# Kernel optimization log

Measured on AMD Instinct MI355X. Metric: run time of the kernel, lower is better.

## Reference

```python
import jax, jax.numpy as jnp
import numpy as np

TEMPERATURE = 0.0005

def conv1d(x, w, b):
    # x: [B,Cin,T], w: [Cout,Cin,K], 'same' padding as ConvNorm (pad=(K-1)//2)
    pad = (w.shape[-1] - 1) // 2
    y = jax.lax.conv_general_dilated(x, w, window_strides=(1,), padding=[(pad, pad)],
                                     dimension_numbers=('NCH', 'OIH', 'NCH'))
    return y + b[None, :, None]

def setup_inputs() -> dict:
    key = jax.random.key(0)
    ks = jax.random.split(key, 20)
    B, C_MEL, C_TXT, C_ATT, T1, T2 = 32, 80, 512, 80, 1600, 400
    s = 0.02
    return {
        'queries': jax.random.normal(ks[0], (B, C_MEL, T1), jnp.float32),
        'keys': jax.random.normal(ks[1], (B, C_TXT, T2), jnp.float32),
        'mask': jax.random.randint(ks[2], (B, T2, 1), 0, 2).astype(bool),
        'attn_prior': jax.random.uniform(ks[3], (B, T1, T2), jnp.float32),
        'speaker_embed': jax.random.normal(ks[4], (B, C_TXT), jnp.float32),
        # key_proj: Conv(512->1024,k3) -> ReLU -> Conv(1024->80,k1)
        'Wk1': jax.random.normal(ks[5], (C_TXT * 2, C_TXT, 3)) * s,
        'bk1': jax.random.normal(ks[6], (C_TXT * 2,)) * s,
        'Wk2': jax.random.normal(ks[7], (C_ATT, C_TXT * 2, 1)) * s,
        'bk2': jax.random.normal(ks[8], (C_ATT,)) * s,
        # query_proj: Conv(80->160,k3) -> ReLU -> Conv(160->80,k1) -> ReLU -> Conv(80->80,k1)
        'Wq1': jax.random.normal(ks[9], (C_MEL * 2, C_MEL, 3)) * s,
        'bq1': jax.random.normal(ks[10], (C_MEL * 2,)) * s,
        'Wq2': jax.random.normal(ks[11], (C_MEL, C_MEL * 2, 1)) * s,
        'bq2': jax.random.normal(ks[12], (C_MEL,)) * s,
        'Wq3': jax.random.normal(ks[13], (C_ATT, C_MEL, 1)) * s,
        'bq3': jax.random.normal(ks[14], (C_ATT,)) * s,
        # speaker projections (multi_speaker=True)
        'Wks': jax.random.normal(ks[15], (C_TXT, C_TXT)) * s,
        'bks': jax.random.normal(ks[16], (C_TXT,)) * s,
        'Wqs': jax.random.normal(ks[17], (C_MEL, C_TXT)) * s,
        'bqs': jax.random.normal(ks[18], (C_MEL,)) * s,
    }

def reference(queries, keys, mask, attn_prior, speaker_embed,
              Wk1, bk1, Wk2, bk2, Wq1, bq1, Wq2, bq2, Wq3, bq3,
              Wks, bks, Wqs, bqs):
    # speaker conditioning: Linear(spk) broadcast over time, added channelwise
    keys = keys + (speaker_embed @ Wks.T + bks)[:, :, None]
    queries = queries + (speaker_embed @ Wqs.T + bqs)[:, :, None]
    # projections
    k = jax.nn.relu(conv1d(keys, Wk1, bk1))
    k = conv1d(k, Wk2, bk2)                      # [B, C_att, T2]
    q = jax.nn.relu(conv1d(queries, Wq1, bq1))
    q = jax.nn.relu(conv1d(q, Wq2, bq2))
    q = conv1d(q, Wq3, bq3)                      # [B, C_att, T1]
    # -temp * sum_c (q-k)^2 == -temp * (||q||^2 + ||k||^2 - 2 q.k)
    q2 = jnp.sum(q * q, axis=1)                  # [B, T1]
    k2 = jnp.sum(k * k, axis=1)                  # [B, T2]
    qk = jnp.einsum('bct,bcs->bts', q, k)        # [B, T1, T2]
    attn = -TEMPERATURE * (q2[:, :, None] + k2[:, None, :] - 2.0 * qk)
    attn = attn[:, None]                         # [B, 1, T1, T2]
    attn = jax.nn.log_softmax(attn, axis=3) + jnp.log(attn_prior[:, None] + 1e-8)
    attn_logprob = attn
    m = jnp.transpose(mask, (0, 2, 1))[:, :, None, :]  # [B,1,1,T2]
    attn = jnp.where(m, -jnp.inf, attn)
    attn = jax.nn.softmax(attn, axis=3)
    return attn, attn_logprob
```

## Files before the change

kernel.cpp:

```cpp
#include <hip/hip_runtime.h>
#include <math.h>

#define TEMP 0.0005f
#define B_    32
#define CMEL  80
#define CTXT  512
#define T1_   1600
#define T2_   400

typedef short short8 __attribute__((ext_vector_type(8)));
typedef float f32x4 __attribute__((ext_vector_type(4)));

__device__ inline unsigned short f2bf(float f) {
    unsigned u = __float_as_uint(f);
    u += 0x7FFF + ((u >> 16) & 1);
    return (unsigned short)(u >> 16);
}
__device__ inline unsigned pack2(float a, float b) {
    return (unsigned)f2bf(a) | ((unsigned)f2bf(b) << 16);
}
__device__ inline float bf2f(unsigned short v) { return __uint_as_float(((unsigned)v) << 16); }

__global__ void bias_kernel(const float* __restrict__ se,
                            const float* __restrict__ Wks, const float* __restrict__ bks,
                            const float* __restrict__ Wqs, const float* __restrict__ bqs,
                            float* __restrict__ kb, float* __restrict__ qb) {
    int tid = blockIdx.x * blockDim.x + threadIdx.x;
    const int nk = B_ * CTXT;
    if (tid < nk) {
        int b = tid / CTXT, c = tid % CTXT;
        const float4* s4 = reinterpret_cast<const float4*>(se + b * CTXT);
        const float4* w4 = reinterpret_cast<const float4*>(Wks + (size_t)c * CTXT);
        float acc = bks[c];
        #pragma unroll 4
        for (int j = 0; j < CTXT / 4; ++j) {
            float4 a = s4[j], w = w4[j];
            acc += a.x * w.x + a.y * w.y + a.z * w.z + a.w * w.w;
        }
        kb[tid] = acc;
    } else if (tid < nk + B_ * CMEL) {
        int t = tid - nk;
        int b = t / CMEL, c = t % CMEL;
        const float4* s4 = reinterpret_cast<const float4*>(se + b * CTXT);
        const float4* w4 = reinterpret_cast<const float4*>(Wqs + (size_t)c * CTXT);
        float acc = bqs[c];
        #pragma unroll 4
        for (int j = 0; j < CTXT / 4; ++j) {
            float4 a = s4[j], w = w4[j];
            acc += a.x * w.x + a.y * w.y + a.z * w.z + a.w * w.w;
        }
        qb[t] = acc;
    }
}

__global__ void cast_weights_kernel(
        const float* __restrict__ Wk1, const float* __restrict__ Wk2,
        const float* __restrict__ Wq1, const float* __restrict__ Wq2,
        const float* __restrict__ Wq3,
        unsigned short* __restrict__ Ab1, unsigned short* __restrict__ A2,
        unsigned short* __restrict__ A3, unsigned short* __restrict__ A4,
        unsigned short* __restrict__ A5) {
    int e = blockIdx.x * 256 + threadIdx.x;
    const int n1 = 1572864, n2 = 81920, n3 = 46080, n4 = 12800, n5 = 7680;
    if (e < n1) {
        int co = e / 1536, rem = e - co * 1536;
        int dt = rem >> 9, ci = rem & 511;
        Ab1[e] = f2bf(Wk1[((size_t)co * 512 + ci) * 3 + dt]);
    } else if ((e -= n1) < n2) {
        A2[e] = f2bf(Wk2[e]);
    } else if ((e -= n2) < n3) {
        int co = e / 288, rem = e - co * 288;
        int dt = rem / 96, cc = rem - dt * 96;
        A3[e] = (cc < 80) ? f2bf(Wq1[((size_t)co * 80 + cc) * 3 + dt]) : 0;
    } else if ((e -= n3) < n4) {
        A4[e] = f2bf(Wq2[e]);
    } else if ((e -= n4) < n5) {
        int co = e / 96, cc = e - co * 96;
        A5[e] = (cc < 80) ? f2bf(Wq3[co * 80 + cc]) : 0;
    }
}

__global__ void castXk_kernel(const float* __restrict__ keys, const float* __restrict__ kb,
                              unsigned short* __restrict__ Xt) {
    __shared__ float tile[64][65];
    const int b = blockIdx.z;
    const int row0 = blockIdx.x * 64;
    const int ci0 = blockIdx.y * 64;
    const int tid = threadIdx.x;
    #pragma unroll
    for (int i = 0; i < 16; ++i) {
        int linear = i * 256 + tid;
        int ci_l = linear >> 6, t_l = linear & 63;
        int t = row0 + t_l - 1;
        float v = 0.f;
        if (t >= 0 && t < 400)
            v = keys[((size_t)b * 512 + ci0 + ci_l) * 400 + t] + kb[b * 512 + ci0 + ci_l];
        tile[t_l][ci_l] = v;
    }
    __syncthreads();
    #pragma unroll
    for (int i = 0; i < 16; ++i) {
        int linear = i * 256 + tid;
        int t_l = linear >> 6, ci_l = linear & 63;
        int row = row0 + t_l;
        if (row < 456)
            Xt[((size_t)b * 456 + row) * 512 + ci0 + ci_l] = f2bf(tile[t_l][ci_l]);
    }
}

__global__ __launch_bounds__(256) void castXq_kernel(
        const float* __restrict__ q, const float* __restrict__ qb,
        unsigned short* __restrict__ Xq1) {
    __shared__ float tile[80][65];
    const int b = blockIdx.y;
    const int t0 = blockIdx.x * 64;
    const int tid = threadIdx.x;
    if (t0 == 0 && tid < 48)
        ((unsigned*)(Xq1 + (size_t)b * 1602 * 96))[tid] = 0u;
    if (t0 == 1536 && tid < 48)
        ((unsigned*)(Xq1 + ((size_t)b * 1602 + 1601) * 96))[tid] = 0u;
    {
        int tl = tid & 63, c0 = tid >> 6;
        for (int c = c0; c < 80; c += 4)
            tile[c][tl] = q[((size_t)b * 80 + c) * 1600 + t0 + tl] + qb[b * 80 + c];
    }
    __syncthreads();
    int row = tid >> 2, cg = tid & 3;
    int t = t0 + row;
    unsigned* orow = (unsigned*)(Xq1 + ((size_t)b * 1602 + t + 1) * 96 + cg * 24);
    #pragma unroll
    for (int jj = 0; jj < 12; ++jj) {
        int c0 = cg * 24 + jj * 2, c1 = c0 + 1;
        float f0 = (c0 < 80) ? tile[c0][row] : 0.f;
        float f1 = (c1 < 80) ? tile[c1][row] : 0.f;
        orow[jj] = pack2(f0, f1);
    }
}

__global__ __launch_bounds__(256) void conv1k_mfma(
        const unsigned short* __restrict__ Ab, const unsigned short* __restrict__ Xt,
        const float* __restrict__ bias, unsigned short* __restrict__ k1c) {
    __shared__ short As[3 * 128 * 40];
    __shared__ short Xs[66 * 40];
    const int b = blockIdx.z;
    const int co0 = blockIdx.y * 128;
    const int t0 = blockIdx.x * 64;
    const int tid = threadIdx.x;
    const int lane = tid & 63, w = tid >> 6;
    const int wm = w >> 1, wn = w & 1;
    const int l15 = lane & 15, quad = lane >> 4;
    f32x4 acc[4][2];
    #pragma unroll
    for (int mt = 0; mt < 4; ++mt)
        #pragma unroll
        for (int nt = 0; nt < 2; ++nt)
            acc[mt][nt] = (f32x4){0.f, 0.f, 0.f, 0.f};

    for (int ci0 = 0; ci0 < 512; ci0 += 32) {
        __syncthreads();
        #pragma unroll
        for (int i = 0; i < 6; ++i) {
            int linear = i * 256 + tid;
            int dt = linear >> 9;
            int rem = linear & 511;
            int r = rem >> 2, c16 = rem & 3;
            int4 v = *(const int4*)(Ab + (size_t)(co0 + r) * 1536 + dt * 512 + ci0 + c16 * 8);
            *(int4*)(As + (dt * 128 + r) * 40 + c16 * 8) = v;
        }
        #pragma unroll
        for (int i = 0; i < 2; ++i) {
            int c = i * 256 + tid;
            if (c < 264) {
                int row = c >> 2, c16 = c & 3;
                int4 v = *(const int4*)(Xt + ((size_t)b * 456 + t0 + row) * 512 + ci0 + c16 * 8);
                *(int4*)(Xs + row * 40 + c16 * 8) = v;
            }
        }
        __syncthreads();
        #pragma unroll
        for (int dt = 0; dt < 3; ++dt) {
            short8 af[4], bfr[2];
            #pragma unroll
            for (int mt = 0; mt < 4; ++mt)
                af[mt] = *(const short8*)(As + (dt * 128 + wm * 64 + mt * 16 + l15) * 40 + quad * 8);
            #pragma unroll
            for (int nt = 0; nt < 2; ++nt)
                bfr[nt] = *(const short8*)(Xs + (wn * 32 + nt * 16 + l15 + dt) * 40 + quad * 8);
            #pragma unroll
            for (int mt = 0; mt < 4; ++mt)
                #pragma unroll
                for (int nt = 0; nt < 2; ++nt)
                    acc[mt][nt] = __builtin_amdgcn_mfma_f32_16x16x32_bf16(af[mt], bfr[nt], acc[mt][nt], 0, 0, 0);
        }
    }
    #pragma unroll
    for (int mt = 0; mt < 4; ++mt) {
        int cob = co0 + wm * 64 + mt * 16 + quad * 4;
        float bv[4];
        #pragma unroll
        for (int r = 0; r < 4; ++r) bv[r] = bias[cob + r];
        #pragma unroll
        for (int nt = 0; nt < 2; ++nt) {
            int t = t0 + wn * 32 + nt * 16 + l15;
            if (t >= 400) continue;
            float v0 = fmaxf(acc[mt][nt][0] + bv[0], 0.f);
            float v1 = fmaxf(acc[mt][nt][1] + bv[1], 0.f);
            float v2 = fmaxf(acc[mt][nt][2] + bv[2], 0.f);
            float v3 = fmaxf(acc[mt][nt][3] + bv[3], 0.f);
            uint2 p;
            p.x = pack2(v0, v1);
            p.y = pack2(v2, v3);
            *(uint2*)(k1c + ((size_t)b * 400 + t) * 1024 + cob) = p;
        }
    }
}

template<int MT, int NKC, int DTC, bool RELU, int OMODE, int INW, int OUTW, int N, int NR>
__global__ __launch_bounds__(256) void gemm_cl(
        const unsigned short* __restrict__ A, const unsigned short* __restrict__ X,
        const float* __restrict__ bias, unsigned short* __restrict__ out) {
    const int b = blockIdx.y;
    const int tid = threadIdx.x;
    const int lane = tid & 63, w = tid >> 6;
    const int l15 = lane & 15, quad = lane >> 4;
    const int s = blockIdx.x * 64 + w * 16 + l15;
    const int srow = (s < N) ? s : (N - 1);
    const unsigned short* xb = X + (size_t)b * NR * INW;

    f32x4 acc[MT];
    #pragma unroll
    for (int mt = 0; mt < MT; ++mt) acc[mt] = (f32x4){0.f, 0.f, 0.f, 0.f};

    #pragma unroll
    for (int kc = 0; kc < NKC; ++kc) {
        const int dt = DTC ? (kc / DTC) : 0;
        const int koff = DTC ? ((kc - dt * DTC) * 32) : (kc * 32);
        short8 bfr = *(const short8*)(xb + (size_t)(srow + dt) * INW + koff + quad * 8);
        #pragma unroll
        for (int mt = 0; mt < MT; ++mt) {
            short8 af = *(const short8*)(A + (size_t)(mt * 16 + l15) * (NKC * 32) + kc * 32 + quad * 8);
            acc[mt] = __builtin_amdgcn_mfma_f32_16x16x32_bf16(af, bfr, acc[mt], 0, 0, 0);
        }
    }
    if (s >= N) return;

    float v[MT][4];
    float ss = 0.f;
    #pragma unroll
    for (int mt = 0; mt < MT; ++mt) {
        #pragma unroll
        for (int r = 0; r < 4; ++r) {
            float x = acc[mt][r] + bias[mt * 16 + quad * 4 + r];
            if (RELU) x = fmaxf(x, 0.f);
            v[mt][r] = x;
            if (OMODE >= 2) ss += x * x;
        }
    }
    if (OMODE >= 2) {
        ss += __shfl_xor(ss, 16, 64);
        ss += __shfl_xor(ss, 32, 64);
    }
    unsigned short* orow = out + ((size_t)b * N + s) * OUTW;
    #pragma unroll
    for (int mt = 0; mt < MT; ++mt) {
        uint2 p;
        p.x = pack2(v[mt][0], v[mt][1]);
        p.y = pack2(v[mt][2], v[mt][3]);
        *(uint2*)(orow + mt * 16 + quad * 4) = p;
    }
    if (OMODE == 1 && quad == 0) {
        uint4 z = {0u, 0u, 0u, 0u};
        *(uint4*)(orow + 80) = z;
        *(uint4*)(orow + 88) = z;
    }
    if (OMODE >= 2 && quad == 0) {
        float e80 = (OMODE == 2) ? (-0.5f * ss) : 1.0f;
        float e81 = (OMODE == 2) ? 1.0f : (-0.5f * ss);
        uint4 z0 = {pack2(e80, e81), 0u, 0u, 0u};
        uint4 z1 = {0u, 0u, 0u, 0u};
        *(uint4*)(orow + 80) = z0;
        *(uint4*)(orow + 88) = z1;
    }
}

__global__ __launch_bounds__(64) void attn_logits_kernel(
        const unsigned short* __restrict__ qT, const unsigned short* __restrict__ kT,
        unsigned short* __restrict__ lgt) {
    const int b = blockIdx.y;
    const int t10 = blockIdx.x * 16;
    const int lane = threadIdx.x;
    const int l15 = lane & 15, quad = lane >> 4;

    const unsigned short* qrow = qT + ((size_t)b * T1_ + t10 + l15) * 96;
    short8 af[3];
    #pragma unroll
    for (int kc = 0; kc < 3; ++kc)
        af[kc] = *(const short8*)(qrow + kc * 32 + quad * 8);

    f32x4 acc[25];
    #pragma unroll
    for (int ns = 0; ns < 25; ++ns) acc[ns] = (f32x4){0.f, 0.f, 0.f, 0.f};
    const unsigned short* kbase = kT + (size_t)b * T2_ * 96 + l15 * 96 + quad * 8;
    #pragma unroll
    for (int ns = 0; ns < 25; ++ns) {
        #pragma unroll
        for (int kc = 0; kc < 3; ++kc) {
            short8 bf = *(const short8*)(kbase + ns * 16 * 96 + kc * 32);
            acc[ns] = __builtin_amdgcn_mfma_f32_16x16x32_bf16(af[kc], bf, acc[ns], 0, 0, 0);
        }
    }
    const float K2T = 2.0f * TEMP;
    #pragma unroll
    for (int r = 0; r < 4; ++r) {
        unsigned short* orow = lgt + ((size_t)b * T1_ + t10 + quad * 4 + r) * T2_;
        #pragma unroll
        for (int ns = 0; ns < 25; ++ns)
            orow[ns * 16 + l15] = f2bf(K2T * acc[ns][r]);
    }
}

__global__ __launch_bounds__(256) void softmax_kernel(
        const unsigned short* __restrict__ lgt, const int* __restrict__ mask,
        const float* __restrict__ prior,
        float* __restrict__ attn_out, float* __restrict__ lp_out) {
    const int b = blockIdx.y;
    const int t1 = blockIdx.x * 4 + (threadIdx.x >> 6);
    const int lane = threadIdx.x & 63;
    const unsigned short* lrow = lgt + ((size_t)b * T1_ + t1) * T2_;
    const float* prow = prior + ((size_t)b * T1_ + t1) * T2_;
    const int* mrow = mask + b * T2_;

    float l[7], pe[7], kp[7];
    #pragma unroll
    for (int j = 0; j < 7; ++j) {
        int s = lane + 64 * j;
        bool v = (j < 6) || (lane < 16);
        l[j]  = v ? bf2f(lrow[s]) : -1e30f;
        pe[j] = v ? (prow[s] + 1e-8f) : 1.f;
        kp[j] = (v && !mrow[v ? s : 0]) ? 1.f : 0.f;
    }
    float m = l[0];
    #pragma unroll
    for (int j = 1; j < 7; ++j) m = fmaxf(m, l[j]);
    #pragma unroll
    for (int off = 1; off <= 32; off <<= 1) m = fmaxf(m, __shfl_xor(m, off, 64));
    float e1[7];
    float sum = 0.f;
    #pragma unroll
    for (int j = 0; j < 7; ++j) { float e = __expf(l[j] - m); e1[j] = e; sum += e; }
    #pragma unroll
    for (int off = 1; off <= 32; off <<= 1) sum += __shfl_xor(sum, off, 64);
    const float lse = m + __logf(sum);

    float u[7];
    float sum2 = 0.f;
    #pragma unroll
    for (int j = 0; j < 7; ++j) {
        float uu = e1[j] * pe[j] * kp[j];
        u[j] = uu;
        sum2 += uu;
    }
    #pragma unroll
    for (int off = 1; off <= 32; off <<= 1) sum2 += __shfl_xor(sum2, off, 64);
    const float inv = 1.f / sum2;

    float* lpr = lp_out + ((size_t)b * T1_ + t1) * T2_;
    float* atr = attn_out + ((size_t)b * T1_ + t1) * T2_;
    #pragma unroll
    for (int j = 0; j < 7; ++j) {
        int s = lane + 64 * j;
        bool v = (j < 6) || (lane < 16);
        if (v) {
            lpr[s] = l[j] - lse + __logf(pe[j]);
            atr[s] = u[j] * inv;
        }
    }
}

extern "C" void kernel_launch(void* const* d_in, const int* in_sizes, int n_in,
                              void* d_out, int out_size, void* d_ws, size_t ws_size,
                              hipStream_t stream) {
    const float* queries = (const float*)d_in[0];
    const float* keys    = (const float*)d_in[1];
    const int*   mask    = (const int*)d_in[2];
    const float* prior   = (const float*)d_in[3];
    const float* se      = (const float*)d_in[4];
    const float* Wk1 = (const float*)d_in[5];
    const float* bk1 = (const float*)d_in[6];
    const float* Wk2 = (const float*)d_in[7];
    const float* bk2 = (const float*)d_in[8];
    const float* Wq1 = (const float*)d_in[9];
    const float* bq1 = (const float*)d_in[10];
    const float* Wq2 = (const float*)d_in[11];
    const float* bq2 = (const float*)d_in[12];
    const float* Wq3 = (const float*)d_in[13];
    const float* bq3 = (const float*)d_in[14];
    const float* Wks = (const float*)d_in[15];
    const float* bks = (const float*)d_in[16];
    const float* Wqs = (const float*)d_in[17];
    const float* bqs = (const float*)d_in[18];

    float* ws = (float*)d_ws;
    float* kb = ws;
    float* qb = ws + 16384;
    unsigned short* Ab1 = (unsigned short*)(ws + 18944);
    unsigned short* A2  = (unsigned short*)(ws + 805376);
    unsigned short* A3  = (unsigned short*)(ws + 846336);
    unsigned short* A4  = (unsigned short*)(ws + 869376);
    unsigned short* A5  = (unsigned short*)(ws + 875776);
    unsigned short* qT  = (unsigned short*)(ws + 879616);
    unsigned short* kT  = (unsigned short*)(ws + 3337216);
    const size_t D = 3951616;
    unsigned short* Xk  = (unsigned short*)(ws + D);
    unsigned short* k1c = (unsigned short*)(ws + D + 3735552);
    unsigned short* Xq1 = (unsigned short*)(ws + D);
    unsigned short* Xq2 = (unsigned short*)(ws + D + 2460672);
    unsigned short* Xq3 = (unsigned short*)(ws + D);
    unsigned short* lgt = (unsigned short*)(ws + D);

    float* attn_out = (float*)d_out;
    float* lp_out   = attn_out + (size_t)B_ * T1_ * T2_;

    bias_kernel<<<dim3(74), dim3(256), 0, stream>>>(se, Wks, bks, Wqs, bqs, kb, qb);
    cast_weights_kernel<<<dim3(6724), dim3(256), 0, stream>>>(Wk1, Wk2, Wq1, Wq2, Wq3,
                                                              Ab1, A2, A3, A4, A5);
    castXk_kernel<<<dim3(8, 8, 32), dim3(256), 0, stream>>>(keys, kb, Xk);
    conv1k_mfma<<<dim3(7, 8, 32), dim3(256), 0, stream>>>(Ab1, Xk, bk1, k1c);
    gemm_cl<5, 32, 0, false, 2, 1024, 96, 400, 400>
        <<<dim3(7, 32), 256, 0, stream>>>(A2, k1c, bk2, kT);
    castXq_kernel<<<dim3(25, 32), dim3(256), 0, stream>>>(queries, qb, Xq1);
    gemm_cl<10, 9, 3, true, 0, 96, 160, 1600, 1602>
        <<<dim3(25, 32), 256, 0, stream>>>(A3, Xq1, bq1, Xq2);
    gemm_cl<5, 5, 0, true, 1, 160, 96, 1600, 1600>
        <<<dim3(25, 32), 256, 0, stream>>>(A4, Xq2, bq2, Xq3);
    gemm_cl<5, 3, 0, false, 3, 96, 96, 1600, 1600>
        <<<dim3(25, 32), 256, 0, stream>>>(A5, Xq3, bq3, qT);
    attn_logits_kernel<<<dim3(100, 32), dim3(64), 0, stream>>>(qT, kT, lgt);
    softmax_kernel<<<dim3(400, 32), dim3(256), 0, stream>>>(lgt, mask, prior, attn_out, lp_out);
}
```

Before: 519.8 us.

## Split-K the key projection GEMM across waves and merge prep kernels

Replaces the generic gemm_cl launch for the 1024->80 key projection, which used only 7x32 blocks, with a dedicated kernel. It launches 25x32 blocks of 16 columns, has four waves each compute a quarter of the K dimension, and reduces their partials through shared memory. The epilogue still writes the squared-norm and constant columns. The bias and weight-cast kernels are also fused into one launch to remove one kernel launch. The cost is extra shared-memory traffic and a barrier, and three of the four waves sit idle during the epilogue.

Result: no change. 514.1 us (-1.1%).

```diff
diff --git a/kernel.cpp b/kernel.cpp
--- a/kernel.cpp
+++ b/kernel.cpp
@@ -21,46 +21,46 @@
 }
 __device__ inline float bf2f(unsigned short v) { return __uint_as_float(((unsigned)v) << 16); }
 
-__global__ void bias_kernel(const float* __restrict__ se,
+__global__ void prep_kernel(const float* __restrict__ se,
                             const float* __restrict__ Wks, const float* __restrict__ bks,
                             const float* __restrict__ Wqs, const float* __restrict__ bqs,
-                            float* __restrict__ kb, float* __restrict__ qb) {
-    int tid = blockIdx.x * blockDim.x + threadIdx.x;
-    const int nk = B_ * CTXT;
-    if (tid < nk) {
-        int b = tid / CTXT, c = tid % CTXT;
-        const float4* s4 = reinterpret_cast<const float4*>(se + b * CTXT);
-        const float4* w4 = reinterpret_cast<const float4*>(Wks + (size_t)c * CTXT);
-        float acc = bks[c];
-        #pragma unroll 4
-        for (int j = 0; j < CTXT / 4; ++j) {
-            float4 a = s4[j], w = w4[j];
-            acc += a.x * w.x + a.y * w.y + a.z * w.z + a.w * w.w;
-        }
-        kb[tid] = acc;
-    } else if (tid < nk + B_ * CMEL) {
-        int t = tid - nk;
-        int b = t / CMEL, c = t % CMEL;
-        const float4* s4 = reinterpret_cast<const float4*>(se + b * CTXT);
-        const float4* w4 = reinterpret_cast<const float4*>(Wqs + (size_t)c * CTXT);
-        float acc = bqs[c];
-        #pragma unroll 4
-        for (int j = 0; j < CTXT / 4; ++j) {
-            float4 a = s4[j], w = w4[j];
-            acc += a.x * w.x + a.y * w.y + a.z * w.z + a.w * w.w;
-        }
-        qb[t] = acc;
-    }
-}
-
-__global__ void cast_weights_kernel(
-        const float* __restrict__ Wk1, const float* __restrict__ Wk2,
-        const float* __restrict__ Wq1, const float* __restrict__ Wq2,
-        const float* __restrict__ Wq3,
-        unsigned short* __restrict__ Ab1, unsigned short* __restrict__ A2,
-        unsigned short* __restrict__ A3, unsigned short* __restrict__ A4,
-        unsigned short* __restrict__ A5) {
-    int e = blockIdx.x * 256 + threadIdx.x;
+                            float* __restrict__ kb, float* __restrict__ qb,
+                            const float* __restrict__ Wk1, const float* __restrict__ Wk2,
+                            const float* __restrict__ Wq1, const float* __restrict__ Wq2,
+                            const float* __restrict__ Wq3,
+                            unsigned short* __restrict__ Ab1, unsigned short* __restrict__ A2,
+                            unsigned short* __restrict__ A3, unsigned short* __restrict__ A4,
+                            unsigned short* __restrict__ A5) {
+    if (blockIdx.x < 74) {
+        int tid = blockIdx.x * blockDim.x + threadIdx.x;
+        const int nk = B_ * CTXT;
+        if (tid < nk) {
+            int b = tid / CTXT, c = tid % CTXT;
+            const float4* s4 = reinterpret_cast<const float4*>(se + b * CTXT);
+            const float4* w4 = reinterpret_cast<const float4*>(Wks + (size_t)c * CTXT);
+            float acc = bks[c];
+            #pragma unroll 4
+            for (int j = 0; j < CTXT / 4; ++j) {
+                float4 a = s4[j], w = w4[j];
+                acc += a.x * w.x + a.y * w.y + a.z * w.z + a.w * w.w;
+            }
+            kb[tid] = acc;
+        } else if (tid < nk + B_ * CMEL) {
+            int t = tid - nk;
+            int b = t / CMEL, c = t % CMEL;
+            const float4* s4 = reinterpret_cast<const float4*>(se + b * CTXT);
+            const float4* w4 = reinterpret_cast<const float4*>(Wqs + (size_t)c * CTXT);
+            float acc = bqs[c];
+            #pragma unroll 4
+            for (int j = 0; j < CTXT / 4; ++j) {
+                float4 a = s4[j], w = w4[j];
+                acc += a.x * w.x + a.y * w.y + a.z * w.z + a.w * w.w;
+            }
+            qb[t] = acc;
+        }
+        return;
+    }
+    int e = (blockIdx.x - 74) * 256 + threadIdx.x;
     const int n1 = 1572864, n2 = 81920, n3 = 46080, n4 = 12800, n5 = 7680;
     if (e < n1) {
         int co = e / 1536, rem = e - co * 1536;
@@ -277,6 +277,72 @@
         float e80 = (OMODE == 2) ? (-0.5f * ss) : 1.0f;
         float e81 = (OMODE == 2) ? 1.0f : (-0.5f * ss);
         uint4 z0 = {pack2(e80, e81), 0u, 0u, 0u};
+        uint4 z1 = {0u, 0u, 0u, 0u};
+        *(uint4*)(orow + 80) = z0;
+        *(uint4*)(orow + 88) = z1;
+    }
+}
+
+__global__ __launch_bounds__(256) void gemm_k2_kernel(
+        const unsigned short* __restrict__ A, const unsigned short* __restrict__ X,
+        const float* __restrict__ bias, unsigned short* __restrict__ out) {
+    __shared__ float red[3][64][21];
+    const int b = blockIdx.y;
+    const int tid = threadIdx.x, lane = tid & 63, w = tid >> 6;
+    const int l15 = lane & 15, quad = lane >> 4;
+    const int s = blockIdx.x * 16 + l15;
+    const unsigned short* xb = X + ((size_t)b * 400 + s) * 1024 + quad * 8;
+    f32x4 acc[5];
+    #pragma unroll
+    for (int mt = 0; mt < 5; ++mt) acc[mt] = (f32x4){0.f, 0.f, 0.f, 0.f};
+    #pragma unroll
+    for (int kk = 0; kk < 8; ++kk) {
+        int kc = w * 8 + kk;
+        short8 bfr = *(const short8*)(xb + kc * 32);
+        #pragma unroll
+        for (int mt = 0; mt < 5; ++mt) {
+            short8 af = *(const short8*)(A + (size_t)(mt * 16 + l15) * 1024 + kc * 32 + quad * 8);
+            acc[mt] = __builtin_amdgcn_mfma_f32_16x16x32_bf16(af, bfr, acc[mt], 0, 0, 0);
+        }
+    }
+    if (w > 0) {
+        #pragma unroll
+        for (int mt = 0; mt < 5; ++mt)
+            #pragma unroll
+            for (int r = 0; r < 4; ++r)
+                red[w - 1][lane][mt * 4 + r] = acc[mt][r];
+    }
+    __syncthreads();
+    if (w != 0) return;
+    #pragma unroll
+    for (int wv = 0; wv < 3; ++wv)
+        #pragma unroll
+        for (int mt = 0; mt < 5; ++mt)
+            #pragma unroll
+            for (int r = 0; r < 4; ++r)
+                acc[mt][r] += red[wv][lane][mt * 4 + r];
+    float v[5][4];
+    float ss = 0.f;
+    #pragma unroll
+    for (int mt = 0; mt < 5; ++mt)
+        #pragma unroll
+        for (int r = 0; r < 4; ++r) {
+            float x = acc[mt][r] + bias[mt * 16 + quad * 4 + r];
+            v[mt][r] = x;
+            ss += x * x;
+        }
+    ss += __shfl_xor(ss, 16, 64);
+    ss += __shfl_xor(ss, 32, 64);
+    unsigned short* orow = out + ((size_t)b * 400 + s) * 96;
+    #pragma unroll
+    for (int mt = 0; mt < 5; ++mt) {
+        uint2 p;
+        p.x = pack2(v[mt][0], v[mt][1]);
+        p.y = pack2(v[mt][2], v[mt][3]);
+        *(uint2*)(orow + mt * 16 + quad * 4) = p;
+    }
+    if (quad == 0) {
+        uint4 z0 = {pack2(-0.5f * ss, 1.0f), 0u, 0u, 0u};
         uint4 z1 = {0u, 0u, 0u, 0u};
         *(uint4*)(orow + 80) = z0;
         *(uint4*)(orow + 88) = z1;
@@ -421,13 +487,12 @@
     float* attn_out = (float*)d_out;
     float* lp_out   = attn_out + (size_t)B_ * T1_ * T2_;
 
-    bias_kernel<<<dim3(74), dim3(256), 0, stream>>>(se, Wks, bks, Wqs, bqs, kb, qb);
-    cast_weights_kernel<<<dim3(6724), dim3(256), 0, stream>>>(Wk1, Wk2, Wq1, Wq2, Wq3,
-                                                              Ab1, A2, A3, A4, A5);
+    prep_kernel<<<dim3(6798), dim3(256), 0, stream>>>(se, Wks, bks, Wqs, bqs, kb, qb,
+                                                      Wk1, Wk2, Wq1, Wq2, Wq3,
+                                                      Ab1, A2, A3, A4, A5);
     castXk_kernel<<<dim3(8, 8, 32), dim3(256), 0, stream>>>(keys, kb, Xk);
     conv1k_mfma<<<dim3(7, 8, 32), dim3(256), 0, stream>>>(Ab1, Xk, bk1, k1c);
-    gemm_cl<5, 32, 0, false, 2, 1024, 96, 400, 400>
-        <<<dim3(7, 32), 256, 0, stream>>>(A2, k1c, bk2, kT);
+    gemm_k2_kernel<<<dim3(25, 32), 256, 0, stream>>>(A2, k1c, bk2, kT);
     castXq_kernel<<<dim3(25, 32), dim3(256), 0, stream>>>(queries, qb, Xq1);
     gemm_cl<10, 9, 3, true, 0, 96, 160, 1600, 1602>
         <<<dim3(25, 32), 256, 0, stream>>>(A3, Xq1, bq1, Xq2);
```
